# Kernel tuning notes

Hardware: AMD Instinct MI355X
Metric: run time of the kernel (lower is better)

Reference implementation:

```python
import jax, jax.numpy as jnp
import numpy as np

HEAD_DIM = 64
N_HEADS = 16


def _rope_tables(seq_len, head_dim):
    pos = np.arange(seq_len, dtype=np.float32)
    freq = np.arange(0, head_dim, 2, dtype=np.float32) / head_dim
    inv_freq = 1.0 / (10000.0 ** freq)
    angles = np.outer(pos, inv_freq)                     # [S, D/2]
    angles = np.repeat(angles, 2, axis=-1)               # [S, D] interleaved
    return jnp.asarray(np.cos(angles)), jnp.asarray(np.sin(angles))


def _rotate_half(x):
    x1 = x[..., ::2]
    x2 = x[..., 1::2]
    return jnp.stack((-x2, x1), axis=-1).reshape(x.shape)


def _apply_rope(x, cos, sin):
    # x: [B, H, S, D]; cos/sin: [S, D]
    return x * cos + _rotate_half(x) * sin


def setup_inputs() -> dict:
    key = jax.random.key(0)
    ks = jax.random.split(key, 5)
    d = N_HEADS * HEAD_DIM
    B, S = 4, 2048
    s = 1.0 / np.sqrt(d)
    return {
        "x": jax.random.normal(ks[0], (B, S, d), dtype=jnp.float32),
        "Wq": jax.random.normal(ks[1], (d, d), dtype=jnp.float32) * s,
        "bq": jnp.zeros((d,), jnp.float32),
        "Wk": jax.random.normal(ks[2], (d, d), dtype=jnp.float32) * s,
        "bk": jnp.zeros((d,), jnp.float32),
        "Wv": jax.random.normal(ks[3], (d, d), dtype=jnp.float32) * s,
        "bv": jnp.zeros((d,), jnp.float32),
        "Wo": jax.random.normal(ks[4], (d, d), dtype=jnp.float32) * s,
        "bo": jnp.zeros((d,), jnp.float32),
    }


def reference(x, Wq, bq, Wk, bk, Wv, bv, Wo, bo):
    B, S, d = x.shape
    H, D = N_HEADS, HEAD_DIM
    scale = D ** -0.5

    q = (x @ Wq + bq).reshape(B, S, H, D).transpose(0, 2, 1, 3)  # [B,H,S,D]
    k = (x @ Wk + bk).reshape(B, S, H, D).transpose(0, 2, 1, 3)
    v = (x @ Wv + bv).reshape(B, S, H, D).transpose(0, 2, 1, 3)

    cos, sin = _rope_tables(S, D)
    q = _apply_rope(q, cos, sin)
    k = _apply_rope(k, cos, sin)

    att = jnp.einsum("bhqd,bhkd->bhqk", q, k) * scale            # [B,H,S,S]
    causal = jnp.tril(jnp.ones((S, S), dtype=bool))
    att = jnp.where(causal, att, -jnp.inf)
    att = jax.nn.softmax(att, axis=-1)

    y = jnp.einsum("bhqk,bhkd->bhqd", att, v)                    # [B,H,S,D]
    y = y.transpose(0, 2, 1, 3).reshape(B, S, d)
    return y @ Wo + bo
```

## Files before the change

### kernel.cpp

```cpp
#include <hip/hip_runtime.h>

typedef __bf16 bf16;
typedef __bf16 bf16x2 __attribute__((ext_vector_type(2)));
typedef __bf16 bf16x4 __attribute__((ext_vector_type(4)));
typedef __bf16 bf16x8 __attribute__((ext_vector_type(8)));
typedef float  f32x4  __attribute__((ext_vector_type(4)));

#define MFMA16(a,b,c) __builtin_amdgcn_mfma_f32_16x16x32_bf16(a,b,c,0,0,0)
#define GLL16(g, l) __builtin_amdgcn_global_load_lds( \
    (const __attribute__((address_space(1))) unsigned char*)(g), \
    (__attribute__((address_space(3))) unsigned char*)(l), 16, 0, 0)
#define BARRIER() asm volatile("s_barrier" ::: "memory")
#define DRAIN(n)  asm volatile("s_waitcnt vmcnt(" #n ")" ::: "memory")

constexpr int SEQ   = 2048;
constexpr int NH    = 16;
constexpr int HD    = 64;
constexpr int BATCH = 4;
constexpr int DM    = 1024;
constexpr size_t TEN = (size_t)BATCH * NH * SEQ * HD;

__global__ __launch_bounds__(256) void k_prep(const float* __restrict__ x,
                                              const float* __restrict__ W0,
                                              const float* __restrict__ W1,
                                              const float* __restrict__ W2,
                                              const float* __restrict__ W3,
                                              bf16* __restrict__ Wt_all,
                                              bf16* __restrict__ xb) {
    __shared__ float T[64][65];
    const int z = blockIdx.z;
    const int t = threadIdx.x;
    if (z == 4) {
        const int bi = blockIdx.y * 16 + blockIdx.x;
#pragma unroll
        for (int c = 0; c < 16; c++) {
            const size_t idx = (size_t)c * 524288 + ((size_t)bi * 256 + t) * 8;
            float4 f0 = *(const float4*)(x + idx);
            float4 f1 = *(const float4*)(x + idx + 4);
            bf16x8 o;
            o[0] = (bf16)f0.x; o[1] = (bf16)f0.y; o[2] = (bf16)f0.z; o[3] = (bf16)f0.w;
            o[4] = (bf16)f1.x; o[5] = (bf16)f1.y; o[6] = (bf16)f1.z; o[7] = (bf16)f1.w;
            *(bf16x8*)(xb + idx) = o;
        }
        return;
    }
    const float* W = (z == 0) ? W0 : (z == 1) ? W1 : (z == 2) ? W2 : W3;
    bf16* Wt = Wt_all + (size_t)z * DM * DM;
    const int kb = blockIdx.x, nb = blockIdx.y;
    const int rl = t >> 2, seg = t & 3;
    const float* src = W + (size_t)(kb * 64 + rl) * DM + nb * 64 + seg * 16;
#pragma unroll
    for (int j4 = 0; j4 < 4; j4++) {
        float4 f = *(const float4*)(src + j4 * 4);
        T[rl][seg * 16 + j4 * 4 + 0] = f.x;
        T[rl][seg * 16 + j4 * 4 + 1] = f.y;
        T[rl][seg * 16 + j4 * 4 + 2] = f.z;
        T[rl][seg * 16 + j4 * 4 + 3] = f.w;
    }
    __syncthreads();
    bf16* dst = Wt + (size_t)(nb * 64 + rl) * DM + kb * 64 + seg * 16;
    bf16x8 o0, o1;
#pragma unroll
    for (int j = 0; j < 8; j++) {
        o0[j] = (bf16)T[seg * 16 + j][rl];
        o1[j] = (bf16)T[seg * 16 + 8 + j][rl];
    }
    *(bf16x8*)dst = o0;
    *(bf16x8*)(dst + 8) = o1;
}

template <int MODE>
__global__ __launch_bounds__(512, 1) void k_gemm(const bf16* __restrict__ A,
                                                 const bf16* __restrict__ Wt0,
                                                 const float* __restrict__ b0,
                                                 const float* __restrict__ b1,
                                                 const float* __restrict__ b2,
                                                 bf16* __restrict__ vt,
                                                 void* __restrict__ out) {
    __shared__ __align__(1024) bf16 LA[3][16384];
    __shared__ __align__(1024) bf16 LB[2][8192];
    const int t = threadIdx.x;
    const int w = t >> 6, lane = t & 63, quad = lane >> 4, l16 = lane & 15;
    const int bm = blockIdx.x * 256;
    const int by = blockIdx.y;
    const int z  = (MODE == 0) ? (by >> 3) : 0;
    const int bn = (MODE == 0) ? ((by & 7) * 128) : (by * 128);
    const bf16* Wt = Wt0 + (size_t)z * DM * DM;
    const float* bias = (z == 0) ? b0 : (z == 1) ? b1 : b2;
    const int wm = (w >> 1) * 64, wn = (w & 1) * 64;

    const int srow = lane >> 3;
    const int sseg = (lane & 7) ^ srow;
    const bf16* gA = A  + (size_t)(bm + w * 8 + srow) * DM + sseg * 8;
    const bf16* gB = Wt + (size_t)(bn + w * 8 + srow) * DM + sseg * 8;

#define STGA_P(lp, tt, c) do { \
    const bf16* _g = gA + (size_t)(c) * 128 * DM + (size_t)(tt) * 64; \
    bf16* _l = (lp) + ((c) * 16 + w) * 512; \
    GLL16(_g, _l); GLL16(_g + 64 * DM, _l + 4096); \
} while (0)
#define STGB_P(lp, tt) do { \
    const bf16* _g = gB + (size_t)(tt) * 64; \
    bf16* _l = (lp) + w * 512; \
    GLL16(_g, _l); GLL16(_g + 64 * DM, _l + 4096); \
} while (0)

    const int sA0 = (quad ^ (l16 & 7)) << 3;
    const int sA1 = ((4 + quad) ^ (l16 & 7)) << 3;

    f32x4 zero = {0.f, 0.f, 0.f, 0.f};
    f32x4 acc[4][4];
#pragma unroll
    for (int mt = 0; mt < 4; mt++)
#pragma unroll
        for (int nt = 0; nt < 4; nt++) acc[mt][nt] = zero;
    bf16x8 bfr[4][2];

#define PH(la_, lb_, mb, READB, STAGE_STMT, DRAIN_STMT) do { \
    const bf16* _la = (la_); \
    if (READB) { \
        const bf16* _lb = (lb_); \
        _Pragma("unroll") \
        for (int nt = 0; nt < 4; nt++) { \
            const int r = (wn + nt * 16 + l16) * 64; \
            bfr[nt][0] = *(const bf16x8*)(_lb + r + sA0); \
            bfr[nt][1] = *(const bf16x8*)(_lb + r + sA1); \
        } \
    } \
    bf16x8 af[2][2]; \
    _Pragma("unroll") \
    for (int mi = 0; mi < 2; mi++) { \
        const int r = (wm + ((mb) + mi) * 16 + l16) * 64; \
        af[mi][0] = *(const bf16x8*)(_la + r + sA0); \
        af[mi][1] = *(const bf16x8*)(_la + r + sA1); \
    } \
    STAGE_STMT; \
    DRAIN_STMT; \
    BARRIER(); \
    __builtin_amdgcn_s_setprio(1); \
    _Pragma("unroll") \
    for (int mi = 0; mi < 2; mi++) \
        _Pragma("unroll") \
        for (int nt = 0; nt < 4; nt++) { \
            f32x4 a = acc[(mb) + mi][nt]; \
            a = MFMA16(af[mi][0], bfr[nt][0], a); \
            a = MFMA16(af[mi][1], bfr[nt][1], a); \
            acc[(mb) + mi][nt] = a; \
        } \
    __builtin_amdgcn_s_setprio(0); \
    BARRIER(); \
} while (0)

    STGA_P(&LA[0][0], 0, 0); STGA_P(&LA[0][0], 0, 1); STGB_P(&LB[0][0], 0);
    STGA_P(&LA[1][0], 1, 0); STGA_P(&LA[1][0], 1, 1); STGB_P(&LB[1][0], 1);
    DRAIN(6);
    BARRIER();

    int ae = 0, ao = 1, an = 2;
    for (int i = 0; i < 8; i++) {
        const int tE = (i < 7) ? 2 * i + 2 : 15;
        const int tO = (i < 7) ? 2 * i + 3 : 15;
        bf16* lae = &LA[0][0] + ae * 16384;
        bf16* lao = &LA[0][0] + ao * 16384;
        bf16* lan = &LA[0][0] + an * 16384;
        PH(lae, &LB[0][0], 0, 1, { STGA_P(lan, tE, 0); STGA_P(lan, tE, 1); }, );
        PH(lae, (const bf16*)0, 2, 0, STGB_P(&LB[0][0], tE), DRAIN(6));
        PH(lao, &LB[1][0], 0, 1, { STGA_P(lae, tO, 0); STGA_P(lae, tO, 1); }, );
        PH(lao, (const bf16*)0, 2, 0, STGB_P(&LB[1][0], tO), DRAIN(6));
        const int tmp = ae; ae = an; an = ao; ao = tmp;
    }
#undef PH
#undef STGA_P
#undef STGB_P

    float bv[4], invf[4];
#pragma unroll
    for (int nt = 0; nt < 4; nt++) {
        const int col = bn + wn + nt * 16 + l16;
        bv[nt] = bias[col];
        if (MODE == 0) {
            const int ip = (col & 63) >> 1;
            invf[nt] = __builtin_exp2f(-0.41524101186092029f * (float)ip);
        }
    }
    const int odd = l16 & 1;

    if (MODE == 0 && z == 2) {
#pragma unroll
        for (int mt = 0; mt < 4; mt++) {
            const int row0 = bm + wm + mt * 16 + quad * 4;
            const int b = row0 >> 11, s0 = row0 & (SEQ - 1);
#pragma unroll
            for (int nt = 0; nt < 4; nt++) {
                const int col = bn + wn + nt * 16 + l16;
                const int h = col >> 6, dd = col & 63;
                bf16x4 o;
#pragma unroll
                for (int rg = 0; rg < 4; rg++) o[rg] = (bf16)(acc[mt][nt][rg] + bv[nt]);
                *(bf16x4*)(vt + ((size_t)((b * NH + h) * HD + dd)) * SEQ + s0) = o;
            }
        }
        return;
    }

#pragma unroll
    for (int mt = 0; mt < 4; mt++) {
#pragma unroll
        for (int nt = 0; nt < 4; nt++) {
            const int col = bn + wn + nt * 16 + l16;
#pragma unroll
            for (int rg = 0; rg < 4; rg++) {
                const int row = bm + wm + mt * 16 + quad * 4 + rg;
                float val = acc[mt][nt][rg] + bv[nt];
                if (MODE == 0) {
                    const int b = row >> 11, s = row & (SEQ - 1);
                    const int h = col >> 6, dd = col & 63;
                    const float partner = __shfl_xor(val, 1);
                    float sn, cs;
                    __sincosf((float)s * invf[nt], &sn, &cs);
                    val = odd ? (val * cs + partner * sn)
                              : (val * cs - partner * sn);
                    if (z == 0) val *= 0.125f;
                    ((bf16*)out)[(size_t)z * TEN +
                                 (((size_t)(b * NH + h)) * SEQ + s) * HD + dd] = (bf16)val;
                } else {
                    ((float*)out)[(size_t)row * DM + col] = val;
                }
            }
        }
    }
}

__global__ __launch_bounds__(256, 3) void k_attn(const bf16* __restrict__ q,
                                                 const bf16* __restrict__ k,
                                                 const bf16* __restrict__ vt,
                                                 bf16* __restrict__ y) {
    __shared__ __align__(1024) bf16 KsF[2][4096];
    __shared__ __align__(1024) bf16 VsF[2][4096];
    __shared__ __align__(1024) bf16 PsF[4 * 32 * 64];
    const int t = threadIdx.x;
    const int w = t >> 6, lane = t & 63, quad = lane >> 4, l16 = lane & 15;
    const int bh = blockIdx.x;
    const int qb = 15 - (int)blockIdx.y;
    const int b = bh >> 4, h = bh & 15;

    const int srow = lane >> 3;
    const int gseg = (lane & 7) ^ srow;
    const int c0 = w, c1 = w + 4;

    const bf16* kbase = k  + (size_t)bh * SEQ * HD;
    const bf16* vbase = vt + (size_t)bh * HD * SEQ;
    const float NEG_INF = -__builtin_inff();

    const int koff0 = (c0 * 8 + srow) * HD + gseg * 8;
    const int koff1 = (c1 * 8 + srow) * HD + gseg * 8;
    const int voff0 = (c0 * 8 + srow) * SEQ + gseg * 8;
    const int voff1 = (c1 * 8 + srow) * SEQ + gseg * 8;

#define STGKV(buf, tt) do { \
    GLL16(kbase + (size_t)(tt) * 64 * HD + koff0, &KsF[buf][c0 * 512]); \
    GLL16(kbase + (size_t)(tt) * 64 * HD + koff1, &KsF[buf][c1 * 512]); \
    GLL16(vbase + (size_t)(tt) * 64 + voff0, &VsF[buf][c0 * 512]); \
    GLL16(vbase + (size_t)(tt) * 64 + voff1, &VsF[buf][c1 * 512]); \
} while (0)

    bf16x8 qf[2][2];
#pragma unroll
    for (int mt = 0; mt < 2; mt++) {
        const bf16* qrow = q + ((size_t)bh * SEQ + qb * 128 + w * 32 + mt * 16 + l16) * HD;
        qf[mt][0] = *(const bf16x8*)(qrow + quad * 8);
        qf[mt][1] = *(const bf16x8*)(qrow + 32 + quad * 8);
    }

    const int ktmax = 2 * qb + 1;
    STGKV(0, 0);
    STGKV(1, 1);

    int off_kv[4][2];
#pragma unroll
    for (int nt = 0; nt < 4; nt++) {
        const int r = nt * 16 + l16;
#pragma unroll
        for (int hh = 0; hh < 2; hh++) {
            const int sg = hh * 4 + quad;
            off_kv[nt][hh] = r * 64 + ((sg ^ (r & 7)) << 3);
        }
    }
    const bf16 *pf_p[2][2];
#pragma unroll
    for (int mt = 0; mt < 2; mt++) {
        const int r = mt * 16 + l16;
#pragma unroll
        for (int hh = 0; hh < 2; hh++) {
            const int sg = hh * 4 + quad;
            pf_p[mt][hh] = PsF + w * 2048 + r * 64 + ((sg ^ (r & 7)) << 3);
        }
    }

    f32x4 zero = {0.f, 0.f, 0.f, 0.f};
    f32x4 minus10 = {-10.f, -10.f, -10.f, -10.f};
    f32x4 acc_o[2][4];
    float l_acc[2][4];
#pragma unroll
    for (int mt = 0; mt < 2; mt++)
#pragma unroll
        for (int nt = 0; nt < 4; nt++) acc_o[mt][nt] = zero;
#pragma unroll
    for (int mt = 0; mt < 2; mt++)
#pragma unroll
        for (int rg = 0; rg < 4; rg++) l_acc[mt][rg] = 0.f;

    DRAIN(4);
    BARRIER();

    for (int kt = 0; kt <= ktmax; kt++) {
        const int cur = kt & 1;
        const bf16* kb_ = &KsF[0][0] + cur * 4096;
        const bf16* vb_ = &VsF[0][0] + cur * 4096;

        const int d = qb * 128 + w * 32 - kt * 64;
        if (d > -32) {
            f32x4 accs[2][4];
            __builtin_amdgcn_s_setprio(1);
#pragma unroll
            for (int nt = 0; nt < 4; nt++) {
                const bf16x8 kf0 = *(const bf16x8*)(kb_ + off_kv[nt][0]);
                const bf16x8 kf1 = *(const bf16x8*)(kb_ + off_kv[nt][1]);
#pragma unroll
                for (int mt = 0; mt < 2; mt++) {
                    f32x4 a = minus10;
                    a = MFMA16(qf[mt][0], kf0, a);
                    a = MFMA16(qf[mt][1], kf1, a);
                    accs[mt][nt] = a;
                }
            }
            __builtin_amdgcn_s_setprio(0);
            if (d < 64) {
#pragma unroll
                for (int mt = 0; mt < 2; mt++) {
                    const int qr = d + mt * 16 + quad * 4;
#pragma unroll
                    for (int nt = 0; nt < 4; nt++) {
                        const int kv = nt * 16 + l16;
#pragma unroll
                        for (int rg = 0; rg < 4; rg++)
                            if (kv > qr + rg) accs[mt][nt][rg] = NEG_INF;
                    }
                }
            }
#pragma unroll
            for (int mt = 0; mt < 2; mt++) {
#pragma unroll
                for (int nt = 0; nt < 4; nt++) {
#pragma unroll
                    for (int rg = 0; rg < 4; rg++) {
                        const float p = __expf(accs[mt][nt][rg]);
                        l_acc[mt][rg] += p;
                        const int prow = mt * 16 + quad * 4 + rg;
                        const int psg  = (nt * 2 + (l16 >> 3)) ^ (prow & 7);
                        PsF[w * 2048 + prow * 64 + psg * 8 + (l16 & 7)] = (bf16)p;
                    }
                }
            }
            bf16x8 pf[2][2];
#pragma unroll
            for (int mt = 0; mt < 2; mt++) {
                pf[mt][0] = *(const bf16x8*)pf_p[mt][0];
                pf[mt][1] = *(const bf16x8*)pf_p[mt][1];
            }
            __builtin_amdgcn_s_setprio(1);
#pragma unroll
            for (int nt = 0; nt < 4; nt++) {
                const bf16x8 vf0 = *(const bf16x8*)(vb_ + off_kv[nt][0]);
                const bf16x8 vf1 = *(const bf16x8*)(vb_ + off_kv[nt][1]);
#pragma unroll
                for (int mt = 0; mt < 2; mt++) {
                    acc_o[mt][nt] = MFMA16(pf[mt][0], vf0, acc_o[mt][nt]);
                    acc_o[mt][nt] = MFMA16(pf[mt][1], vf1, acc_o[mt][nt]);
                }
            }
            __builtin_amdgcn_s_setprio(0);
        }
        if (kt < ktmax) {
            BARRIER();
            const int ts = (kt + 2 > ktmax) ? ktmax : (kt + 2);
            STGKV(cur, ts);
            DRAIN(4);
            BARRIER();
        }
    }
#undef STGKV

#pragma unroll
    for (int mt = 0; mt < 2; mt++) {
#pragma unroll
        for (int rg = 0; rg < 4; rg++) {
            float rs = l_acc[mt][rg];
            rs += __shfl_xor(rs, 1);
            rs += __shfl_xor(rs, 2);
            rs += __shfl_xor(rs, 4);
            rs += __shfl_xor(rs, 8);
            const float inv = 1.0f / rs;
            const int s = qb * 128 + w * 32 + mt * 16 + quad * 4 + rg;
#pragma unroll
            for (int nt = 0; nt < 4; nt++) {
                const float val = acc_o[mt][nt][rg] * inv;
                y[((size_t)(b * SEQ + s)) * DM + h * HD + nt * 16 + l16] = (bf16)val;
            }
        }
    }
}

extern "C" void kernel_launch(void* const* d_in, const int* in_sizes, int n_in,
                              void* d_out, int out_size, void* d_ws, size_t ws_size,
                              hipStream_t stream) {
    const float* x  = (const float*)d_in[0];
    const float* Wq = (const float*)d_in[1];
    const float* bq = (const float*)d_in[2];
    const float* Wk = (const float*)d_in[3];
    const float* bk = (const float*)d_in[4];
    const float* Wv = (const float*)d_in[5];
    const float* bv = (const float*)d_in[6];
    const float* Wo = (const float*)d_in[7];
    const float* bo = (const float*)d_in[8];

    char* ws = (char*)d_ws;
    bf16* xb   = (bf16*)(ws);
    bf16* wall = (bf16*)(ws + (16ull << 20));
    bf16* qb   = (bf16*)(ws + (24ull << 20));
    bf16* kb   = (bf16*)(ws + (40ull << 20));
    bf16* vtb  = (bf16*)(ws + (72ull << 20));
    bf16* wot  = wall + 3ull * DM * DM;

    k_prep<<<dim3(16, 16, 5), 256, 0, stream>>>(x, Wq, Wk, Wv, Wo, wall, xb);
    k_gemm<0><<<dim3(32, 24), 512, 0, stream>>>(xb, wall, bq, bk, bv, vtb, qb);
    k_attn<<<dim3(64, 16), 256, 0, stream>>>(qb, kb, vtb, xb);
    k_gemm<1><<<dim3(32, 8), 512, 0, stream>>>(xb, wot, bo, bo, bo, vtb, d_out);
}
```

Measured before the change: 239.4 us.

## Split attention block into 8 waves of 16 query rows each

The attention kernel now runs 512 threads per block, and each of 8 waves owns 16 query rows instead of 4 waves owning 32. Per-wave register state for Q fragments, accumulators and P tiles is halved, and each wave issues one K and one V async load per tile instead of two. The aim is more resident waves to hide LDS and memory latency and finer-grained causal skipping. The cost is half the MFMA work per K/V fragment read from LDS, plus more barrier participants per block.

```diff
diff --git a/kernel.cpp b/kernel.cpp
--- a/kernel.cpp
+++ b/kernel.cpp
@@ -231,13 +231,13 @@
     }
 }
 
-__global__ __launch_bounds__(256, 3) void k_attn(const bf16* __restrict__ q,
+__global__ __launch_bounds__(512, 4) void k_attn(const bf16* __restrict__ q,
                                                  const bf16* __restrict__ k,
                                                  const bf16* __restrict__ vt,
                                                  bf16* __restrict__ y) {
     __shared__ __align__(1024) bf16 KsF[2][4096];
     __shared__ __align__(1024) bf16 VsF[2][4096];
-    __shared__ __align__(1024) bf16 PsF[4 * 32 * 64];
+    __shared__ __align__(1024) bf16 PsF[8 * 16 * 64];
     const int t = threadIdx.x;
     const int w = t >> 6, lane = t & 63, quad = lane >> 4, l16 = lane & 15;
     const int bh = blockIdx.x;
@@ -246,30 +246,24 @@
 
     const int srow = lane >> 3;
     const int gseg = (lane & 7) ^ srow;
-    const int c0 = w, c1 = w + 4;
 
     const bf16* kbase = k  + (size_t)bh * SEQ * HD;
     const bf16* vbase = vt + (size_t)bh * HD * SEQ;
     const float NEG_INF = -__builtin_inff();
 
-    const int koff0 = (c0 * 8 + srow) * HD + gseg * 8;
-    const int koff1 = (c1 * 8 + srow) * HD + gseg * 8;
-    const int voff0 = (c0 * 8 + srow) * SEQ + gseg * 8;
-    const int voff1 = (c1 * 8 + srow) * SEQ + gseg * 8;
+    const int koff = (w * 8 + srow) * HD + gseg * 8;
+    const int voff = (w * 8 + srow) * SEQ + gseg * 8;
 
 #define STGKV(buf, tt) do { \
-    GLL16(kbase + (size_t)(tt) * 64 * HD + koff0, &KsF[buf][c0 * 512]); \
-    GLL16(kbase + (size_t)(tt) * 64 * HD + koff1, &KsF[buf][c1 * 512]); \
-    GLL16(vbase + (size_t)(tt) * 64 + voff0, &VsF[buf][c0 * 512]); \
-    GLL16(vbase + (size_t)(tt) * 64 + voff1, &VsF[buf][c1 * 512]); \
+    GLL16(kbase + (size_t)(tt) * 64 * HD + koff, &KsF[buf][w * 512]); \
+    GLL16(vbase + (size_t)(tt) * 64 + voff, &VsF[buf][w * 512]); \
 } while (0)
 
-    bf16x8 qf[2][2];
-#pragma unroll
-    for (int mt = 0; mt < 2; mt++) {
-        const bf16* qrow = q + ((size_t)bh * SEQ + qb * 128 + w * 32 + mt * 16 + l16) * HD;
-        qf[mt][0] = *(const bf16x8*)(qrow + quad * 8);
-        qf[mt][1] = *(const bf16x8*)(qrow + 32 + quad * 8);
+    bf16x8 qf[2];
+    {
+        const bf16* qrow = q + ((size_t)bh * SEQ + qb * 128 + w * 16 + l16) * HD;
+        qf[0] = *(const bf16x8*)(qrow + quad * 8);
+        qf[1] = *(const bf16x8*)(qrow + 32 + quad * 8);
     }
 
     const int ktmax = 2 * qb + 1;
@@ -286,31 +280,23 @@
             off_kv[nt][hh] = r * 64 + ((sg ^ (r & 7)) << 3);
         }
     }
-    const bf16 *pf_p[2][2];
-#pragma unroll
-    for (int mt = 0; mt < 2; mt++) {
-        const int r = mt * 16 + l16;
-#pragma unroll
-        for (int hh = 0; hh < 2; hh++) {
-            const int sg = hh * 4 + quad;
-            pf_p[mt][hh] = PsF + w * 2048 + r * 64 + ((sg ^ (r & 7)) << 3);
-        }
+    const bf16 *pf_p[2];
+#pragma unroll
+    for (int hh = 0; hh < 2; hh++) {
+        const int sg = hh * 4 + quad;
+        pf_p[hh] = PsF + w * 1024 + l16 * 64 + ((sg ^ (l16 & 7)) << 3);
     }
 
     f32x4 zero = {0.f, 0.f, 0.f, 0.f};
     f32x4 minus10 = {-10.f, -10.f, -10.f, -10.f};
-    f32x4 acc_o[2][4];
-    float l_acc[2][4];
-#pragma unroll
-    for (int mt = 0; mt < 2; mt++)
-#pragma unroll
-        for (int nt = 0; nt < 4; nt++) acc_o[mt][nt] = zero;
-#pragma unroll
-    for (int mt = 0; mt < 2; mt++)
-#pragma unroll
-        for (int rg = 0; rg < 4; rg++) l_acc[mt][rg] = 0.f;
-
-    DRAIN(4);
+    f32x4 acc_o[4];
+    float l_acc[4];
+#pragma unroll
+    for (int nt = 0; nt < 4; nt++) acc_o[nt] = zero;
+#pragma unroll
+    for (int rg = 0; rg < 4; rg++) l_acc[rg] = 0.f;
+
+    DRAIN(2);
     BARRIER();
 
     for (int kt = 0; kt <= ktmax; kt++) {
@@ -318,66 +304,50 @@
         const bf16* kb_ = &KsF[0][0] + cur * 4096;
         const bf16* vb_ = &VsF[0][0] + cur * 4096;
 
-        const int d = qb * 128 + w * 32 - kt * 64;
-        if (d > -32) {
-            f32x4 accs[2][4];
+        const int d = qb * 128 + w * 16 - kt * 64;
+        if (d > -16) {
+            f32x4 accs[4];
             __builtin_amdgcn_s_setprio(1);
 #pragma unroll
             for (int nt = 0; nt < 4; nt++) {
                 const bf16x8 kf0 = *(const bf16x8*)(kb_ + off_kv[nt][0]);
                 const bf16x8 kf1 = *(const bf16x8*)(kb_ + off_kv[nt][1]);
-#pragma unroll
-                for (int mt = 0; mt < 2; mt++) {
-                    f32x4 a = minus10;
-                    a = MFMA16(qf[mt][0], kf0, a);
-                    a = MFMA16(qf[mt][1], kf1, a);
-                    accs[mt][nt] = a;
-                }
+                f32x4 a = minus10;
+                a = MFMA16(qf[0], kf0, a);
+                a = MFMA16(qf[1], kf1, a);
+                accs[nt] = a;
             }
             __builtin_amdgcn_s_setprio(0);
             if (d < 64) {
-#pragma unroll
-                for (int mt = 0; mt < 2; mt++) {
-                    const int qr = d + mt * 16 + quad * 4;
-#pragma unroll
-                    for (int nt = 0; nt < 4; nt++) {
-                        const int kv = nt * 16 + l16;
-#pragma unroll
-                        for (int rg = 0; rg < 4; rg++)
-                            if (kv > qr + rg) accs[mt][nt][rg] = NEG_INF;
-                    }
+                const int qr = d + quad * 4;
+#pragma unroll
+                for (int nt = 0; nt < 4; nt++) {
+                    const int kv = nt * 16 + l16;
+#pragma unroll
+                    for (int rg = 0; rg < 4; rg++)
+                        if (kv > qr + rg) accs[nt][rg] = NEG_INF;
                 }
             }
 #pragma unroll
-            for (int mt = 0; mt < 2; mt++) {
-#pragma unroll
-                for (int nt = 0; nt < 4; nt++) {
-#pragma unroll
-                    for (int rg = 0; rg < 4; rg++) {
-                        const float p = __expf(accs[mt][nt][rg]);
-                        l_acc[mt][rg] += p;
-                        const int prow = mt * 16 + quad * 4 + rg;
-                        const int psg  = (nt * 2 + (l16 >> 3)) ^ (prow & 7);
-                        PsF[w * 2048 + prow * 64 + psg * 8 + (l16 & 7)] = (bf16)p;
-                    }
+            for (int nt = 0; nt < 4; nt++) {
+#pragma unroll
+                for (int rg = 0; rg < 4; rg++) {
+                    const float p = __expf(accs[nt][rg]);
+                    l_acc[rg] += p;
+                    const int prow = quad * 4 + rg;
+                    const int psg  = (nt * 2 + (l16 >> 3)) ^ (prow & 7);
+                    PsF[w * 1024 + prow * 64 + psg * 8 + (l16 & 7)] = (bf16)p;
                 }
             }
-            bf16x8 pf[2][2];
-#pragma unroll
-            for (int mt = 0; mt < 2; mt++) {
-                pf[mt][0] = *(const bf16x8*)pf_p[mt][0];
-                pf[mt][1] = *(const bf16x8*)pf_p[mt][1];
-            }
+            bf16x8 pf0 = *(const bf16x8*)pf_p[0];
+            bf16x8 pf1 = *(const bf16x8*)pf_p[1];
             __builtin_amdgcn_s_setprio(1);
 #pragma unroll
             for (int nt = 0; nt < 4; nt++) {
                 const bf16x8 vf0 = *(const bf16x8*)(vb_ + off_kv[nt][0]);
                 const bf16x8 vf1 = *(const bf16x8*)(vb_ + off_kv[nt][1]);
-#pragma unroll
-                for (int mt = 0; mt < 2; mt++) {
-                    acc_o[mt][nt] = MFMA16(pf[mt][0], vf0, acc_o[mt][nt]);
-                    acc_o[mt][nt] = MFMA16(pf[mt][1], vf1, acc_o[mt][nt]);
-                }
+                acc_o[nt] = MFMA16(pf0, vf0, acc_o[nt]);
+                acc_o[nt] = MFMA16(pf1, vf1, acc_o[nt]);
             }
             __builtin_amdgcn_s_setprio(0);
         }
@@ -385,28 +355,25 @@
             BARRIER();
             const int ts = (kt + 2 > ktmax) ? ktmax : (kt + 2);
             STGKV(cur, ts);
-            DRAIN(4);
+            DRAIN(2);
             BARRIER();
         }
     }
 #undef STGKV
 
 #pragma unroll
-    for (int mt = 0; mt < 2; mt++) {
-#pragma unroll
-        for (int rg = 0; rg < 4; rg++) {
-            float rs = l_acc[mt][rg];
-            rs += __shfl_xor(rs, 1);
-            rs += __shfl_xor(rs, 2);
-            rs += __shfl_xor(rs, 4);
-            rs += __shfl_xor(rs, 8);
-            const float inv = 1.0f / rs;
-            const int s = qb * 128 + w * 32 + mt * 16 + quad * 4 + rg;
-#pragma unroll
-            for (int nt = 0; nt < 4; nt++) {
-                const float val = acc_o[mt][nt][rg] * inv;
-                y[((size_t)(b * SEQ + s)) * DM + h * HD + nt * 16 + l16] = (bf16)val;
-            }
+    for (int rg = 0; rg < 4; rg++) {
+        float rs = l_acc[rg];
+        rs += __shfl_xor(rs, 1);
+        rs += __shfl_xor(rs, 2);
+        rs += __shfl_xor(rs, 4);
+        rs += __shfl_xor(rs, 8);
+        const float inv = 1.0f / rs;
+        const int s = qb * 128 + w * 16 + quad * 4 + rg;
+#pragma unroll
+        for (int nt = 0; nt < 4; nt++) {
+            const float val = acc_o[nt][rg] * inv;
+            y[((size_t)(b * SEQ + s)) * DM + h * HD + nt * 16 + l16] = (bf16)val;
         }
     }
 }
@@ -434,6 +401,6 @@
 
     k_prep<<<dim3(16, 16, 5), 256, 0, stream>>>(x, Wq, Wk, Wv, Wo, wall, xb);
     k_gemm<0><<<dim3(32, 24), 512, 0, stream>>>(xb, wall, bq, bk, bv, vtb, qb);
-    k_attn<<<dim3(64, 16), 256, 0, stream>>>(qb, kb, vtb, xb);
+    k_attn<<<dim3(64, 16), 512, 0, stream>>>(qb, kb, vtb, xb);
     k_gemm<1><<<dim3(32, 8), 512, 0, stream>>>(xb, wot, bo, bo, bo, vtb, d_out);
 }
```

Result: no change. 243.7 us (+1.8%).
